# Optimization experiments

Measured on AMD Instinct MI355X. Metric: run time of the kernel, lower is better.

## Reference

```python
import jax, jax.numpy as jnp
import numpy as np

B, S, D = 2, 2048, 2048
KVH, QPG, HD = 8, 4, 64          # kv heads, q heads per group, head size
THETA = 1024.0
PARTIAL = 0.5
SOFT_CAP = 50.0
EPS = 1e-5


def setup_inputs() -> dict:
    key = jax.random.key(0)
    ks = jax.random.split(key, 8)
    scale = 0.02
    return {
        "x": jax.random.normal(ks[0], (B, S, D), jnp.float32),
        "wq": jax.random.normal(ks[1], (KVH, QPG, HD, D), jnp.float32) * scale,
        "wk": jax.random.normal(ks[2], (KVH, HD, D), jnp.float32) * scale,
        "wv": jax.random.normal(ks[3], (KVH, HD, D), jnp.float32) * scale,
        "wo": jax.random.normal(ks[4], (D, KVH, QPG, HD), jnp.float32) * scale,
        "qn_w": jnp.ones((HD,), jnp.float32),
        "kn_w": jnp.ones((HD,), jnp.float32),
        "pos_ids": jnp.arange(S, dtype=jnp.int32),
    }


def _rms_norm(t, w):
    var = jnp.mean(jnp.square(t), axis=-1, keepdims=True)
    return t * jax.lax.rsqrt(var + EPS) * w


def _rope_tables(pos_ids):
    half = HD // 2
    rotated_size = int(HD * PARTIAL)
    inv_freq = 1.0 / THETA ** (jnp.arange(0, 2 * half, 2, dtype=jnp.float32) / rotated_size)
    inv_freq = jnp.where(jnp.arange(half) < rotated_size // 2, inv_freq, 0.0)
    freqs = pos_ids.astype(jnp.float32)[:, None] * inv_freq[None, :]   # [S, half]
    emb = jnp.concatenate([freqs, freqs], axis=-1)                      # [S, HD]
    return jnp.cos(emb), jnp.sin(emb)


def _apply_rope(t, cos, sin):
    # t: [..., S, HD]; rotate_half: (x1, x2) -> (-x2, x1)
    half = HD // 2
    x1, x2 = t[..., :half], t[..., half:]
    rot = jnp.concatenate([-x2, x1], axis=-1)
    return t * cos + rot * sin


def reference(x, wq, wk, wv, wo, qn_w, kn_w, pos_ids):
    # QKV projections (GQA)
    q = jnp.einsum("bsd,gphd->bgpsh", x, wq)   # [B,KVH,QPG,S,HD]
    k = jnp.einsum("bsd,ghd->bgsh", x, wk)      # [B,KVH,S,HD]
    v = jnp.einsum("bsd,ghd->bgsh", x, wv)

    # QK-norm (RMS over head dim)
    q = _rms_norm(q, qn_w)
    k = _rms_norm(k, kn_w)

    # partial RoPE
    cos, sin = _rope_tables(pos_ids)            # [S, HD]
    q = _apply_rope(q, cos, sin).astype(x.dtype)
    k = _apply_rope(k, cos, sin).astype(x.dtype)

    # attention in fp32 (upcast_attn) with soft cap and causal mask
    scale = 1.0 / jnp.sqrt(jnp.float32(HD))
    scores = jnp.einsum("bgpsh,bgth->bgpst", q.astype(jnp.float32), k.astype(jnp.float32)) * scale
    scores = SOFT_CAP * jnp.tanh(scores / SOFT_CAP)
    causal = pos_ids[:, None] >= pos_ids[None, :]                    # [S, S]
    scores = jnp.where(causal, scores, jnp.finfo(jnp.float32).min)
    probs = jax.nn.softmax(scores, axis=-1)
    attn = jnp.einsum("bgpst,bgth->bgpsh", probs, v.astype(jnp.float32)).astype(x.dtype)

    # output projection (flatten kv_head x q_heads_per_group -> heads)
    out = jnp.einsum("bgpsh,dgph->bsd", attn, wo)
    return out
```

## Files before the change

### kernel.cpp

```cpp
#include <hip/hip_runtime.h>
#include <stdint.h>

#define S_LEN   2048
#define D_MODEL 2048
#define N_KVH   8
#define N_QPG   4
#define N_HD    64

typedef __attribute__((ext_vector_type(8)))  short short8;
typedef __attribute__((ext_vector_type(4)))  short short4v;
typedef __attribute__((ext_vector_type(4)))  float float4v;
typedef __attribute__((ext_vector_type(16))) float floatx16;

__device__ __forceinline__ unsigned short f2bf(float x) {
    unsigned int u = __float_as_uint(x);
    u = (u + 0x7fffu + ((u >> 16) & 1u)) >> 16;
    return (unsigned short)u;
}

__device__ __forceinline__ void gload_lds16(const unsigned short* g, unsigned short* l) {
    __builtin_amdgcn_global_load_lds((const __attribute__((address_space(1))) unsigned int*)g,
                                     (__attribute__((address_space(3))) unsigned int*)l,
                                     16, 0, 0);
}

__global__ __launch_bounds__(256) void cvt_all(const float* __restrict__ x,
                                               const float* __restrict__ wq,
                                               const float* __restrict__ wk,
                                               const float* __restrict__ wv,
                                               const float* __restrict__ wo,
                                               unsigned short* __restrict__ xb,
                                               unsigned short* __restrict__ wqb,
                                               unsigned short* __restrict__ wkb,
                                               unsigned short* __restrict__ wvb,
                                               unsigned short* __restrict__ wob) {
    size_t i = (size_t)blockIdx.x * 256 + threadIdx.x;
    const float* src; unsigned short* dst; size_t off;
    if      (i < 1048576) { src = x;  dst = xb;  off = i; }
    else if (i < 1572864) { src = wq; dst = wqb; off = i - 1048576; }
    else if (i < 1703936) { src = wk; dst = wkb; off = i - 1572864; }
    else if (i < 1835008) { src = wv; dst = wvb; off = i - 1703936; }
    else                  { src = wo; dst = wob; off = i - 1835008; }
    const float4* p = (const float4*)src + off * 2;
    float4 a = p[0], b = p[1];
    union { unsigned short us[8]; uint4 v; } u;
    u.us[0] = f2bf(a.x); u.us[1] = f2bf(a.y); u.us[2] = f2bf(a.z); u.us[3] = f2bf(a.w);
    u.us[4] = f2bf(b.x); u.us[5] = f2bf(b.y); u.us[6] = f2bf(b.z); u.us[7] = f2bf(b.w);
    ((uint4*)dst)[off] = u.v;
}

#define GSTAGE(AL, BL, KO)                         \
    gload_lds16(Ag + (KO),          (AL));         \
    gload_lds16(Ag + 16 * K + (KO), (AL) + 512);   \
    gload_lds16(Bg + (KO),          (BL));         \
    gload_lds16(Bg + 16 * K + (KO), (BL) + 512);

#define GCOMPUTE(OFF)                                                          \
    {                                                                          \
        short8 af[4], bf[4];                                                   \
        _Pragma("unroll")                                                      \
        for (int mt = 0; mt < 4; mt++)                                         \
            af[mt] = *(const short8*)(Alds + (OFF) + (wm + mt * 16 + l15) * 32 + quad * 8); \
        _Pragma("unroll")                                                      \
        for (int nt = 0; nt < 4; nt++)                                         \
            bf[nt] = *(const short8*)(Blds + (OFF) + (wn + nt * 16 + l15) * 32 + quad * 8); \
        _Pragma("unroll")                                                      \
        for (int mt = 0; mt < 4; mt++)                                         \
            _Pragma("unroll")                                                  \
            for (int nt = 0; nt < 4; nt++)                                     \
                acc[mt][nt] = __builtin_amdgcn_mfma_f32_16x16x32_bf16(         \
                    af[mt], bf[nt], acc[mt][nt], 0, 0, 0);                     \
    }

__global__ __launch_bounds__(256)
void gemm_qkv(const unsigned short* __restrict__ xb,
              const unsigned short* __restrict__ wqb,
              const unsigned short* __restrict__ wkb,
              const unsigned short* __restrict__ wvb,
              unsigned short* __restrict__ qout,
              unsigned short* __restrict__ kout,
              unsigned short* __restrict__ vtout,
              const float* __restrict__ qnw,
              const float* __restrict__ knw)
{
    __shared__ __align__(16) unsigned short Alds[2 * 128 * 32];
    __shared__ __align__(16) unsigned short Blds[2 * 128 * 32];

    const int tid  = threadIdx.x;
    const int lane = tid & 63;
    const int wave = tid >> 6;
    const int quad = lane >> 4;
    const int l15  = lane & 15;
    const int bx = blockIdx.x, by = blockIdx.y;
    const int role = (by < 16) ? 0 : (by < 20 ? 1 : 2);
    const unsigned short* A;
    const unsigned short* B;
    int m0, n0;
    if (role == 0)      { A = xb;  B = wqb; m0 = bx * 128; n0 = by * 128; }
    else if (role == 1) { A = xb;  B = wkb; m0 = bx * 128; n0 = (by - 16) * 128; }
    else                { A = wvb; B = xb;  m0 = (by - 20) * 128; n0 = bx * 128; }
    const int K = 2048;
    const int wm = (wave >> 1) * 64;
    const int wn = (wave & 1) * 64;

    float4v acc[4][4];
#pragma unroll
    for (int i = 0; i < 4; i++)
#pragma unroll
        for (int j = 0; j < 4; j++) acc[i][j] = (float4v){0.f, 0.f, 0.f, 0.f};

    const int j0 = wave * 2;
    const int lr = lane >> 2;
    const int lc = (lane & 3) * 8;
    const unsigned short* Ag = A + (size_t)(m0 + j0 * 16 + lr) * K + lc;
    const unsigned short* Bg = B + (size_t)(n0 + j0 * 16 + lr) * K + lc;
    unsigned short* Al0 = Alds + j0 * 512;
    unsigned short* Bl0 = Blds + j0 * 512;
    unsigned short* Al1 = Alds + 4096 + j0 * 512;
    unsigned short* Bl1 = Blds + 4096 + j0 * 512;

    GSTAGE(Al0, Bl0, 0);
    __syncthreads();

    for (int k0 = 0; k0 < K; k0 += 64) {
        GSTAGE(Al1, Bl1, k0 + 32);
        GCOMPUTE(0);
        __syncthreads();
        if (k0 + 64 < K) { GSTAGE(Al0, Bl0, k0 + 64); }
        GCOMPUTE(4096);
        __syncthreads();
    }

    const int nb = n0 + wn;
    const float* nw = (role == 1) ? knw : qnw;
#pragma unroll
    for (int mt = 0; mt < 4; mt++) {
#pragma unroll
        for (int r = 0; r < 4; r++) {
            const int m = m0 + wm + mt * 16 + quad * 4 + r;
            if (role == 2) {
#pragma unroll
                for (int nt = 0; nt < 4; nt++) {
                    int n = nb + nt * 16 + l15;
                    int bb = n >> 11, s = n & 2047;
                    vtout[((((size_t)bb * 8 + (m >> 6)) * 64 + (s >> 5)) * 64 + (m & 63)) * 32 + (s & 31)] =
                        f2bf(acc[mt][nt][r]);
                }
            } else {
                float v0 = acc[mt][0][r], v1 = acc[mt][1][r], v2 = acc[mt][2][r], v3 = acc[mt][3][r];
                float s2 = v0 * v0 + v1 * v1 + v2 * v2 + v3 * v3;
#pragma unroll
                for (int off = 1; off < 16; off <<= 1) s2 += __shfl_xor(s2, off, 64);
                float rs = rsqrtf(s2 * (1.0f / 64.0f) + 1e-5f);
                float nv0 = v0 * rs * nw[0 * 16 + l15];
                float nv1 = v1 * rs * nw[1 * 16 + l15];
                float nv2 = v2 * rs * nw[2 * 16 + l15];
                float nv3 = v3 * rs * nw[3 * 16 + l15];
                const int bidx = m >> 11, s = m & 2047;
                float ang = (float)s * exp2f(-0.625f * (float)l15);
                float sn, cs;
                __sincosf(ang, &sn, &cs);
                float o0 = nv0 * cs - nv2 * sn;
                float o2 = nv2 * cs + nv0 * sn;
                unsigned short* dst;
                if (role == 0) {
                    const int g = nb >> 8, p = (nb >> 6) & 3;
                    dst = qout + ((((size_t)bidx * N_KVH + g) * N_QPG + p) * S_LEN + s) * N_HD;
                } else {
                    const int g = nb >> 6;
                    dst = kout + (((size_t)bidx * N_KVH + g) * S_LEN + s) * N_HD;
                }
                dst[0 * 16 + l15] = f2bf(o0);
                dst[1 * 16 + l15] = f2bf(nv1);
                dst[2 * 16 + l15] = f2bf(o2);
                dst[3 * 16 + l15] = f2bf(nv3);
            }
        }
    }
}

__global__ __launch_bounds__(256)
void gemm_out(const unsigned short* __restrict__ A,
              const unsigned short* __restrict__ B,
              float* __restrict__ C,
              int M, int N, int K)
{
    __shared__ __align__(16) unsigned short Alds[2 * 128 * 32];
    __shared__ __align__(16) unsigned short Blds[2 * 128 * 32];

    const int tid  = threadIdx.x;
    const int lane = tid & 63;
    const int wave = tid >> 6;
    const int quad = lane >> 4;
    const int l15  = lane & 15;
    const int m0 = blockIdx.x * 128;
    const int n0 = blockIdx.y * 128;
    const int wm = (wave >> 1) * 64;
    const int wn = (wave & 1) * 64;

    float4v acc[4][4];
#pragma unroll
    for (int i = 0; i < 4; i++)
#pragma unroll
        for (int j = 0; j < 4; j++) acc[i][j] = (float4v){0.f, 0.f, 0.f, 0.f};

    const int j0 = wave * 2;
    const int lr = lane >> 2;
    const int lc = (lane & 3) * 8;
    const unsigned short* Ag = A + (size_t)(m0 + j0 * 16 + lr) * K + lc;
    const unsigned short* Bg = B + (size_t)(n0 + j0 * 16 + lr) * K + lc;
    unsigned short* Al0 = Alds + j0 * 512;
    unsigned short* Bl0 = Blds + j0 * 512;
    unsigned short* Al1 = Alds + 4096 + j0 * 512;
    unsigned short* Bl1 = Blds + 4096 + j0 * 512;

    GSTAGE(Al0, Bl0, 0);
    __syncthreads();

    for (int k0 = 0; k0 < K; k0 += 64) {
        GSTAGE(Al1, Bl1, k0 + 32);
        GCOMPUTE(0);
        __syncthreads();
        if (k0 + 64 < K) { GSTAGE(Al0, Bl0, k0 + 64); }
        GCOMPUTE(4096);
        __syncthreads();
    }

    const int nb = n0 + wn;
#pragma unroll
    for (int mt = 0; mt < 4; mt++) {
#pragma unroll
        for (int r = 0; r < 4; r++) {
            const int m = m0 + wm + mt * 16 + quad * 4 + r;
#pragma unroll
            for (int nt = 0; nt < 4; nt++) {
                int n = nb + nt * 16 + l15;
                C[(size_t)m * N + n] = acc[mt][nt][r];
            }
        }
    }
}

__global__ __launch_bounds__(512)
void attn_kernel(const unsigned short* __restrict__ Q,
                 const unsigned short* __restrict__ Kb,
                 const unsigned short* __restrict__ Vt,
                 unsigned short* __restrict__ O)
{
    __shared__ float Osc[4 * 32 * 64];
    __shared__ float Rsc[4 * 64];

    const int tid  = threadIdx.x;
    const int lane = tid & 63;
    const int wv   = tid >> 6;
    const int p    = wv & 3;
    const int kvh  = wv >> 2;
    const int l31  = lane & 31;
    const int hi   = lane >> 5;
    const int hi8  = hi * 8;
    const int hi4  = hi * 4;
    const bool lo  = (hi == 0);
    const int qx = blockIdx.y;
    const int bg = blockIdx.x;
    const int b = bg >> 3, g = bg & 7;

    const unsigned short* qbase  = Q  + (((size_t)b * N_KVH + g) * N_QPG + p) * S_LEN * N_HD;
    const unsigned short* kbase  = Kb + ((size_t)b * N_KVH + g) * S_LEN * N_HD;
    const unsigned short* vtbase = Vt + (size_t)bg * (64 * 64 * 32);

    float* OscW = Osc + p * (32 * 64);
    float* RscW = Rsc + p * 64;

    for (int half = 0; half < 2; half++) {
        const int qt = half ? (63 - qx) : qx;
        const int qrow0 = qt * 32;
        const int nkt = qt + 1;
        const int klo = kvh ? (nkt >> 1) : 0;
        const int khi = kvh ? nkt : (nkt >> 1);

        short8 qf[4];
#pragma unroll
        for (int c = 0; c < 4; c++)
            qf[c] = *(const short8*)(qbase + (size_t)(qrow0 + l31) * N_HD + c * 16 + hi8);

        floatx16 o_acc[2];
#pragma unroll
        for (int dt = 0; dt < 2; dt++)
#pragma unroll
            for (int i = 0; i < 16; i++) o_acc[dt][i] = 0.f;
        float rsum = 0.f;

        if (klo < khi) {
            short8 kf[4];
#pragma unroll
            for (int c = 0; c < 4; c++)
                kf[c] = *(const short8*)(kbase + (size_t)(klo * 32 + l31) * N_HD + c * 16 + hi8);

            for (int kt = klo; kt < khi; kt++) {
                floatx16 s;
#pragma unroll
                for (int i = 0; i < 16; i++) s[i] = 0.f;
                __builtin_amdgcn_s_setprio(1);
#pragma unroll
                for (int c = 0; c < 4; c++)
                    s = __builtin_amdgcn_mfma_f32_32x32x16_bf16(kf[c], qf[c], s, 0, 0, 0);
                __builtin_amdgcn_s_setprio(0);

                const unsigned short* tb = vtbase + kt * 2048;
                short8 vf00 = *(const short8*)(tb + l31 * 32 + hi8);
                short8 vf01 = *(const short8*)(tb + l31 * 32 + 16 + hi8);
                short8 vf10 = *(const short8*)(tb + (32 + l31) * 32 + hi8);
                short8 vf11 = *(const short8*)(tb + (32 + l31) * 32 + 16 + hi8);

                if (kt + 1 < khi) {
#pragma unroll
                    for (int c = 0; c < 4; c++)
                        kf[c] = *(const short8*)(kbase + (size_t)((kt + 1) * 32 + l31) * N_HD + c * 16 + hi8);
                }

                const bool diag = (kt == qt);
                float pr[16];
#pragma unroll
                for (int r = 0; r < 16; r++) {
                    float a = s[r];
                    float u = a * a;
                    float wvv = fmaf(u, -3.757018e-7f, 0.18033688f);
                    float pv = __builtin_amdgcn_exp2f(fmaf(a, wvv, -72.13475204f));
                    if (diag) {
                        int kl = (r & 3) + 8 * (r >> 2) + hi4;
                        pv = (kl <= l31) ? pv : 0.0f;
                    }
                    rsum += pv;
                    pr[r] = pv;
                }

                unsigned X0, X1, Y0, Y1, Z0, Z1, W0, W1;
                asm("v_cvt_pk_bf16_f32 %0, %1, %2" : "=v"(X0) : "v"(pr[0]),  "v"(pr[1]));
                asm("v_cvt_pk_bf16_f32 %0, %1, %2" : "=v"(X1) : "v"(pr[2]),  "v"(pr[3]));
                asm("v_cvt_pk_bf16_f32 %0, %1, %2" : "=v"(Y0) : "v"(pr[4]),  "v"(pr[5]));
                asm("v_cvt_pk_bf16_f32 %0, %1, %2" : "=v"(Y1) : "v"(pr[6]),  "v"(pr[7]));
                asm("v_cvt_pk_bf16_f32 %0, %1, %2" : "=v"(Z0) : "v"(pr[8]),  "v"(pr[9]));
                asm("v_cvt_pk_bf16_f32 %0, %1, %2" : "=v"(Z1) : "v"(pr[10]), "v"(pr[11]));
                asm("v_cvt_pk_bf16_f32 %0, %1, %2" : "=v"(W0) : "v"(pr[12]), "v"(pr[13]));
                asm("v_cvt_pk_bf16_f32 %0, %1, %2" : "=v"(W1) : "v"(pr[14]), "v"(pr[15]));
                unsigned sX0 = (unsigned)__shfl_xor((int)X0, 32, 64);
                unsigned sX1 = (unsigned)__shfl_xor((int)X1, 32, 64);
                unsigned sY0 = (unsigned)__shfl_xor((int)Y0, 32, 64);
                unsigned sY1 = (unsigned)__shfl_xor((int)Y1, 32, 64);
                unsigned sZ0 = (unsigned)__shfl_xor((int)Z0, 32, 64);
                unsigned sZ1 = (unsigned)__shfl_xor((int)Z1, 32, 64);
                unsigned sW0 = (unsigned)__shfl_xor((int)W0, 32, 64);
                unsigned sW1 = (unsigned)__shfl_xor((int)W1, 32, 64);
                union { unsigned u[4]; short8 s8; } pb0, pb1;
                pb0.u[0] = lo ? X0  : sY0;
                pb0.u[1] = lo ? X1  : sY1;
                pb0.u[2] = lo ? sX0 : Y0;
                pb0.u[3] = lo ? sX1 : Y1;
                pb1.u[0] = lo ? Z0  : sW0;
                pb1.u[1] = lo ? Z1  : sW1;
                pb1.u[2] = lo ? sZ0 : W0;
                pb1.u[3] = lo ? sZ1 : W1;

                __builtin_amdgcn_s_setprio(1);
                o_acc[0] = __builtin_amdgcn_mfma_f32_32x32x16_bf16(vf00, pb0.s8, o_acc[0], 0, 0, 0);
                o_acc[0] = __builtin_amdgcn_mfma_f32_32x32x16_bf16(vf01, pb1.s8, o_acc[0], 0, 0, 0);
                o_acc[1] = __builtin_amdgcn_mfma_f32_32x32x16_bf16(vf10, pb0.s8, o_acc[1], 0, 0, 0);
                o_acc[1] = __builtin_amdgcn_mfma_f32_32x32x16_bf16(vf11, pb1.s8, o_acc[1], 0, 0, 0);
                __builtin_amdgcn_s_setprio(0);
            }
        }

        __syncthreads();
        if (kvh == 1) {
#pragma unroll
            for (int dt = 0; dt < 2; dt++)
#pragma unroll
                for (int i = 0; i < 16; i++)
                    OscW[(dt * 16 + i) * 64 + lane] = o_acc[dt][i];
            RscW[lane] = rsum;
        }
        __syncthreads();
        if (kvh == 0) {
#pragma unroll
            for (int dt = 0; dt < 2; dt++)
#pragma unroll
                for (int i = 0; i < 16; i++)
                    o_acc[dt][i] += OscW[(dt * 16 + i) * 64 + lane];
            rsum += RscW[lane];

            rsum += __shfl_xor(rsum, 32, 64);
            float inv = 1.0f / rsum;
            size_t rowoff = ((size_t)(b * S_LEN + qrow0 + l31)) * D_MODEL + (g * N_QPG + p) * N_HD;
#pragma unroll
            for (int dt = 0; dt < 2; dt++) {
#pragma unroll
                for (int gg = 0; gg < 4; gg++) {
                    union { unsigned short us[4]; unsigned long long v; } pk;
#pragma unroll
                    for (int j = 0; j < 4; j++)
                        pk.us[j] = f2bf(o_acc[dt][gg * 4 + j] * inv);
                    *(unsigned long long*)(O + rowoff + dt * 32 + gg * 8 + hi4) = pk.v;
                }
            }
        }
    }
}

extern "C" void kernel_launch(void* const* d_in, const int* in_sizes, int n_in,
                              void* d_out, int out_size, void* d_ws, size_t ws_size,
                              hipStream_t stream)
{
    const float* x    = (const float*)d_in[0];
    const float* wq   = (const float*)d_in[1];
    const float* wk   = (const float*)d_in[2];
    const float* wv   = (const float*)d_in[3];
    const float* wo   = (const float*)d_in[4];
    const float* qn_w = (const float*)d_in[5];
    const float* kn_w = (const float*)d_in[6];

    char* ws = (char*)d_ws;
    unsigned short* xb  = (unsigned short*)(ws + 0);
    unsigned short* wqb = (unsigned short*)(ws + 16777216);
    unsigned short* wkb = (unsigned short*)(ws + 25165824);
    unsigned short* wvb = (unsigned short*)(ws + 27262976);
    unsigned short* wob = (unsigned short*)(ws + 29360128);
    unsigned short* qb  = (unsigned short*)(ws + 37748736);
    unsigned short* kb  = (unsigned short*)(ws + 54525952);
    unsigned short* vt  = (unsigned short*)(ws + 58720256);
    unsigned short* ab  = (unsigned short*)(ws + 62914560);

    cvt_all<<<dim3(9216), 256, 0, stream>>>(x, wq, wk, wv, wo, xb, wqb, wkb, wvb, wob);

    gemm_qkv<<<dim3(32, 24), 256, 0, stream>>>(xb, wqb, wkb, wvb, qb, kb, vt, qn_w, kn_w);

    attn_kernel<<<dim3(16, 32), 512, 0, stream>>>(qb, kb, vt, ab);

    gemm_out<<<dim3(32, 16), 256, 0, stream>>>(ab, wob, (float*)d_out, 4096, 2048, 2048);
}
```

Measured before the change: 357.6 us.

## Software-pipeline QK^T MFMA one tile ahead of softmax and PV in attention loop

Restructures the causal attention inner loop so the QK^T score MFMAs for the next key tile are issued before the softmax and PV work of the current tile. It uses double-buffered score accumulators and K fragments, with the loop unrolled by two. The aim is to let the matrix-core work overlap the exp/convert/shuffle VALU work and hide load latency. The extra live accumulators and fragments raise register pressure, which could lower occupancy or cause spills.

```diff
diff --git a/kernel.cpp b/kernel.cpp
--- a/kernel.cpp
+++ b/kernel.cpp
@@ -291,83 +291,108 @@
         float rsum = 0.f;
 
         if (klo < khi) {
-            short8 kf[4];
+            short8 kfA[4], kfB[4];
 #pragma unroll
             for (int c = 0; c < 4; c++)
-                kf[c] = *(const short8*)(kbase + (size_t)(klo * 32 + l31) * N_HD + c * 16 + hi8);
-
-            for (int kt = klo; kt < khi; kt++) {
-                floatx16 s;
-#pragma unroll
-                for (int i = 0; i < 16; i++) s[i] = 0.f;
-                __builtin_amdgcn_s_setprio(1);
+                kfA[c] = *(const short8*)(kbase + (size_t)(klo * 32 + l31) * N_HD + c * 16 + hi8);
+
+            floatx16 sA, sB;
+#pragma unroll
+            for (int i = 0; i < 16; i++) { sA[i] = 0.f; sB[i] = 0.f; }
+            __builtin_amdgcn_s_setprio(1);
+#pragma unroll
+            for (int c = 0; c < 4; c++)
+                sA = __builtin_amdgcn_mfma_f32_32x32x16_bf16(kfA[c], qf[c], sA, 0, 0, 0);
+            __builtin_amdgcn_s_setprio(0);
+
+            if (klo + 1 < khi) {
 #pragma unroll
                 for (int c = 0; c < 4; c++)
-                    s = __builtin_amdgcn_mfma_f32_32x32x16_bf16(kf[c], qf[c], s, 0, 0, 0);
-                __builtin_amdgcn_s_setprio(0);
-
-                const unsigned short* tb = vtbase + kt * 2048;
-                short8 vf00 = *(const short8*)(tb + l31 * 32 + hi8);
-                short8 vf01 = *(const short8*)(tb + l31 * 32 + 16 + hi8);
-                short8 vf10 = *(const short8*)(tb + (32 + l31) * 32 + hi8);
-                short8 vf11 = *(const short8*)(tb + (32 + l31) * 32 + 16 + hi8);
-
-                if (kt + 1 < khi) {
-#pragma unroll
-                    for (int c = 0; c < 4; c++)
-                        kf[c] = *(const short8*)(kbase + (size_t)((kt + 1) * 32 + l31) * N_HD + c * 16 + hi8);
-                }
-
-                const bool diag = (kt == qt);
-                float pr[16];
-#pragma unroll
-                for (int r = 0; r < 16; r++) {
-                    float a = s[r];
-                    float u = a * a;
-                    float wvv = fmaf(u, -3.757018e-7f, 0.18033688f);
-                    float pv = __builtin_amdgcn_exp2f(fmaf(a, wvv, -72.13475204f));
-                    if (diag) {
-                        int kl = (r & 3) + 8 * (r >> 2) + hi4;
-                        pv = (kl <= l31) ? pv : 0.0f;
-                    }
-                    rsum += pv;
-                    pr[r] = pv;
-                }
-
-                unsigned X0, X1, Y0, Y1, Z0, Z1, W0, W1;
-                asm("v_cvt_pk_bf16_f32 %0, %1, %2" : "=v"(X0) : "v"(pr[0]),  "v"(pr[1]));
-                asm("v_cvt_pk_bf16_f32 %0, %1, %2" : "=v"(X1) : "v"(pr[2]),  "v"(pr[3]));
-                asm("v_cvt_pk_bf16_f32 %0, %1, %2" : "=v"(Y0) : "v"(pr[4]),  "v"(pr[5]));
-                asm("v_cvt_pk_bf16_f32 %0, %1, %2" : "=v"(Y1) : "v"(pr[6]),  "v"(pr[7]));
-                asm("v_cvt_pk_bf16_f32 %0, %1, %2" : "=v"(Z0) : "v"(pr[8]),  "v"(pr[9]));
-                asm("v_cvt_pk_bf16_f32 %0, %1, %2" : "=v"(Z1) : "v"(pr[10]), "v"(pr[11]));
-                asm("v_cvt_pk_bf16_f32 %0, %1, %2" : "=v"(W0) : "v"(pr[12]), "v"(pr[13]));
-                asm("v_cvt_pk_bf16_f32 %0, %1, %2" : "=v"(W1) : "v"(pr[14]), "v"(pr[15]));
-                unsigned sX0 = (unsigned)__shfl_xor((int)X0, 32, 64);
-                unsigned sX1 = (unsigned)__shfl_xor((int)X1, 32, 64);
-                unsigned sY0 = (unsigned)__shfl_xor((int)Y0, 32, 64);
-                unsigned sY1 = (unsigned)__shfl_xor((int)Y1, 32, 64);
-                unsigned sZ0 = (unsigned)__shfl_xor((int)Z0, 32, 64);
-                unsigned sZ1 = (unsigned)__shfl_xor((int)Z1, 32, 64);
-                unsigned sW0 = (unsigned)__shfl_xor((int)W0, 32, 64);
-                unsigned sW1 = (unsigned)__shfl_xor((int)W1, 32, 64);
-                union { unsigned u[4]; short8 s8; } pb0, pb1;
-                pb0.u[0] = lo ? X0  : sY0;
-                pb0.u[1] = lo ? X1  : sY1;
-                pb0.u[2] = lo ? sX0 : Y0;
-                pb0.u[3] = lo ? sX1 : Y1;
-                pb1.u[0] = lo ? Z0  : sW0;
-                pb1.u[1] = lo ? Z1  : sW1;
-                pb1.u[2] = lo ? sZ0 : W0;
-                pb1.u[3] = lo ? sZ1 : W1;
-
-                __builtin_amdgcn_s_setprio(1);
-                o_acc[0] = __builtin_amdgcn_mfma_f32_32x32x16_bf16(vf00, pb0.s8, o_acc[0], 0, 0, 0);
-                o_acc[0] = __builtin_amdgcn_mfma_f32_32x32x16_bf16(vf01, pb1.s8, o_acc[0], 0, 0, 0);
-                o_acc[1] = __builtin_amdgcn_mfma_f32_32x32x16_bf16(vf10, pb0.s8, o_acc[1], 0, 0, 0);
-                o_acc[1] = __builtin_amdgcn_mfma_f32_32x32x16_bf16(vf11, pb1.s8, o_acc[1], 0, 0, 0);
-                __builtin_amdgcn_s_setprio(0);
-            }
+                    kfB[c] = *(const short8*)(kbase + (size_t)((klo + 1) * 32 + l31) * N_HD + c * 16 + hi8);
+            }
+
+#define ASTEP(KT, SC, SN, KFN, KFO)                                            \
+            {                                                                  \
+                const int kt_ = (KT);                                          \
+                const unsigned short* tb = vtbase + kt_ * 2048;                \
+                short8 vf00 = *(const short8*)(tb + l31 * 32 + hi8);           \
+                short8 vf01 = *(const short8*)(tb + l31 * 32 + 16 + hi8);      \
+                short8 vf10 = *(const short8*)(tb + (32 + l31) * 32 + hi8);    \
+                short8 vf11 = *(const short8*)(tb + (32 + l31) * 32 + 16 + hi8);\
+                if (kt_ + 1 < khi) {                                           \
+                    _Pragma("unroll")                                          \
+                    for (int i = 0; i < 16; i++) SN[i] = 0.f;                  \
+                    __builtin_amdgcn_s_setprio(1);                             \
+                    _Pragma("unroll")                                          \
+                    for (int c = 0; c < 4; c++)                                \
+                        SN = __builtin_amdgcn_mfma_f32_32x32x16_bf16(          \
+                            KFN[c], qf[c], SN, 0, 0, 0);                       \
+                    __builtin_amdgcn_s_setprio(0);                             \
+                }                                                              \
+                if (kt_ + 2 < khi) {                                           \
+                    _Pragma("unroll")                                          \
+                    for (int c = 0; c < 4; c++)                                \
+                        KFO[c] = *(const short8*)(kbase +                      \
+                            (size_t)((kt_ + 2) * 32 + l31) * N_HD + c * 16 + hi8); \
+                }                                                              \
+                const bool diag = (kt_ == qt);                                 \
+                float pr[16];                                                  \
+                _Pragma("unroll")                                              \
+                for (int r = 0; r < 16; r++) {                                 \
+                    float a = SC[r];                                           \
+                    float u = a * a;                                           \
+                    float wvv = fmaf(u, -3.757018e-7f, 0.18033688f);           \
+                    float pv = __builtin_amdgcn_exp2f(fmaf(a, wvv, -72.13475204f)); \
+                    if (diag) {                                                \
+                        int kl = (r & 3) + 8 * (r >> 2) + hi4;                 \
+                        pv = (kl <= l31) ? pv : 0.0f;                          \
+                    }                                                          \
+                    rsum += pv;                                                \
+                    pr[r] = pv;                                                \
+                }                                                              \
+                unsigned X0, X1, Y0, Y1, Z0, Z1, W0, W1;                       \
+                asm("v_cvt_pk_bf16_f32 %0, %1, %2" : "=v"(X0) : "v"(pr[0]),  "v"(pr[1]));  \
+                asm("v_cvt_pk_bf16_f32 %0, %1, %2" : "=v"(X1) : "v"(pr[2]),  "v"(pr[3]));  \
+                asm("v_cvt_pk_bf16_f32 %0, %1, %2" : "=v"(Y0) : "v"(pr[4]),  "v"(pr[5]));  \
+                asm("v_cvt_pk_bf16_f32 %0, %1, %2" : "=v"(Y1) : "v"(pr[6]),  "v"(pr[7]));  \
+                asm("v_cvt_pk_bf16_f32 %0, %1, %2" : "=v"(Z0) : "v"(pr[8]),  "v"(pr[9]));  \
+                asm("v_cvt_pk_bf16_f32 %0, %1, %2" : "=v"(Z1) : "v"(pr[10]), "v"(pr[11])); \
+                asm("v_cvt_pk_bf16_f32 %0, %1, %2" : "=v"(W0) : "v"(pr[12]), "v"(pr[13])); \
+                asm("v_cvt_pk_bf16_f32 %0, %1, %2" : "=v"(W1) : "v"(pr[14]), "v"(pr[15])); \
+                unsigned sX0 = (unsigned)__shfl_xor((int)X0, 32, 64);          \
+                unsigned sX1 = (unsigned)__shfl_xor((int)X1, 32, 64);          \
+                unsigned sY0 = (unsigned)__shfl_xor((int)Y0, 32, 64);          \
+                unsigned sY1 = (unsigned)__shfl_xor((int)Y1, 32, 64);          \
+                unsigned sZ0 = (unsigned)__shfl_xor((int)Z0, 32, 64);          \
+                unsigned sZ1 = (unsigned)__shfl_xor((int)Z1, 32, 64);          \
+                unsigned sW0 = (unsigned)__shfl_xor((int)W0, 32, 64);          \
+                unsigned sW1 = (unsigned)__shfl_xor((int)W1, 32, 64);          \
+                union { unsigned u[4]; short8 s8; } pb0, pb1;                  \
+                pb0.u[0] = lo ? X0  : sY0;                                     \
+                pb0.u[1] = lo ? X1  : sY1;                                     \
+                pb0.u[2] = lo ? sX0 : Y0;                                      \
+                pb0.u[3] = lo ? sX1 : Y1;                                      \
+                pb1.u[0] = lo ? Z0  : sW0;                                     \
+                pb1.u[1] = lo ? Z1  : sW1;                                     \
+                pb1.u[2] = lo ? sZ0 : W0;                                      \
+                pb1.u[3] = lo ? sZ1 : W1;                                      \
+                __builtin_amdgcn_s_setprio(1);                                 \
+                o_acc[0] = __builtin_amdgcn_mfma_f32_32x32x16_bf16(vf00, pb0.s8, o_acc[0], 0, 0, 0); \
+                o_acc[0] = __builtin_amdgcn_mfma_f32_32x32x16_bf16(vf01, pb1.s8, o_acc[0], 0, 0, 0); \
+                o_acc[1] = __builtin_amdgcn_mfma_f32_32x32x16_bf16(vf10, pb0.s8, o_acc[1], 0, 0, 0); \
+                o_acc[1] = __builtin_amdgcn_mfma_f32_32x32x16_bf16(vf11, pb1.s8, o_acc[1], 0, 0, 0); \
+                __builtin_amdgcn_s_setprio(0);                                 \
+            }
+
+            int kt = klo;
+            while (kt + 1 < khi) {
+                ASTEP(kt,     sA, sB, kfB, kfA);
+                ASTEP(kt + 1, sB, sA, kfA, kfB);
+                kt += 2;
+            }
+            if (kt < khi)
+                ASTEP(kt, sA, sB, kfB, kfA);
+#undef ASTEP
         }
 
         __syncthreads();
```

Result: no change. 356.3 us (-0.4%).
